# Optimization experiments

Measured on AMD Instinct MI355X. Metric: run time of the kernel, lower is better.

The kernel has to match this reference:

```python
import jax, jax.numpy as jnp
import numpy as np

B, N, T, D, O = 8, 1024, 12, 64, 64

def setup_inputs() -> dict:
    key = jax.random.key(0)
    k1, k2, k3 = jax.random.split(key, 3)
    x = jax.random.normal(k1, (B, N, T, D), dtype=jnp.float32)
    # row-normalized random adjacency (dense mask, as in the torch module)
    adj = jax.random.uniform(k2, (N, N), dtype=jnp.float32)
    norm_adj = adj / jnp.sum(adj, axis=-1, keepdims=True)
    theta_w = jax.random.normal(k3, (D, O), dtype=jnp.float32) / np.sqrt(D)
    return {"x": x, "norm_adj": norm_adj, "theta_w": theta_w}

def reference(x, norm_adj, theta_w):
    b, n, t, d = x.shape
    # [B, N, T, D] -> [B*T, N, D]
    xr = jnp.transpose(x, (0, 2, 1, 3)).reshape(b * t, n, d)
    # spatial attention scores [B*T, N, N]
    scores = jnp.einsum('gnd,gmd->gnm', xr, xr) / jnp.sqrt(jnp.float32(d))
    attn = jax.nn.softmax(scores, axis=-1)
    # adjacency-masked attention, then aggregate and project
    agg = jnp.einsum('gnm,gmd->gnd', norm_adj[None, :, :] * attn, xr)
    out = jnp.einsum('gnd,do->gno', agg, theta_w)
    # [B*T, N, O] -> [B, N, T, O], relu
    out = jnp.transpose(out.reshape(b, t, n, -1), (0, 2, 1, 3))
    return jax.nn.relu(out)
```

## Files before the change

kernel.cpp:

```cpp
#include <hip/hip_runtime.h>


#define NB    8
#define NT    12
#define NNODE 1024
#define ND    64
#define XROW  768
#define NG    96

typedef __bf16 bf16x8 __attribute__((ext_vector_type(8)));
typedef __bf16 bf16x4 __attribute__((ext_vector_type(4)));
typedef float  floatx4 __attribute__((ext_vector_type(4)));

#define MFMA(a,b,c) __builtin_amdgcn_mfma_f32_16x16x32_bf16((a),(b),(c),0,0,0)

#define QSCALE 0.18033688011112042f

#define KSTRIDE 72
#define VSTRIDE 40
#define PSTRIDE 36
#define AGSTRIDE 68
#define OFF_KHI 0
#define OFF_KLO 4608
#define OFF_VHI 9216
#define OFF_VLO 14336
#define OFF_P   19456
#define SMEM_BYTES (19456 + 128*PSTRIDE*4)

#define WXHI  0
#define WXLO  6291456
#define WXTHI 12582912
#define WXTLO 18874368
#define WTHI  25165824
#define WTLO  25169920
#define WS_BYTES 50348032ULL

struct bfpair { __bf16 h, l; };

__device__ __forceinline__ bfpair split1(float f) {
    bfpair r;
    __bf16 hb = (__bf16)f;
    float hf = __builtin_bit_cast(float,
                   (unsigned)__builtin_bit_cast(unsigned short, hb) << 16);
    r.h = hb;
    r.l = (__bf16)(f - hf);
    return r;
}

__global__ void __launch_bounds__(256)
presplit(const float* __restrict__ x, const float* __restrict__ theta,
         __bf16* __restrict__ ws)
{
    __shared__ __align__(16) float T[64 * 68];
    const int tid  = threadIdx.x;
    const int bx   = blockIdx.x;
    const int g    = bx >> 4;
    const int nblk = bx & 15;
    const int bb   = g / NT;
    const int tt   = g - bb * NT;
    const int n0   = nblk * 64;

    __bf16* Xhi  = ws + WXHI  + (size_t)g * 65536;
    __bf16* Xlo  = ws + WXLO  + (size_t)g * 65536;
    __bf16* XThi = ws + WXTHI + (size_t)g * 65536;
    __bf16* XTlo = ws + WXTLO + (size_t)g * 65536;
    const float* xg = x + (size_t)bb * (NNODE * XROW) + (size_t)tt * ND;

    #pragma unroll
    for (int i = 0; i < 4; ++i) {
        int chunk = i * 256 + tid;
        int n  = chunk >> 4;
        int c4 = (chunk & 15) * 4;
        floatx4 f = *(const floatx4*)(xg + (size_t)(n0 + n) * XROW + c4);
        *(floatx4*)(T + n * 68 + c4) = f;
        bf16x4 h, l;
        #pragma unroll
        for (int j = 0; j < 4; ++j) {
            bfpair p = split1(f[j]); h[j] = p.h; l[j] = p.l;
        }
        *(bf16x4*)(Xhi + (size_t)(n0 + n) * 64 + c4) = h;
        *(bf16x4*)(Xlo + (size_t)(n0 + n) * 64 + c4) = l;
    }
    __syncthreads();

    {
        const int d  = tid >> 2;
        const int nc = (tid & 3) * 16;
        bf16x8 h0, l0, h1, l1;
        #pragma unroll
        for (int j = 0; j < 8; ++j) {
            bfpair p = split1(T[(nc + j) * 68 + d]);     h0[j] = p.h; l0[j] = p.l;
            bfpair q = split1(T[(nc + 8 + j) * 68 + d]); h1[j] = q.h; l1[j] = q.l;
        }
        __bf16* dsth = XThi + (size_t)d * NNODE + n0 + nc;
        __bf16* dstl = XTlo + (size_t)d * NNODE + n0 + nc;
        *(bf16x8*)dsth = h0; *(bf16x8*)(dsth + 8) = h1;
        *(bf16x8*)dstl = l0; *(bf16x8*)(dstl + 8) = l1;
    }

    if (bx < 2) {
        int c  = bx * 256 + tid;
        int o  = c >> 3;
        int d0 = (c & 7) * 8;
        bf16x8 h, l;
        #pragma unroll
        for (int i = 0; i < 8; ++i) {
            bfpair p = split1(theta[(size_t)(d0 + i) * ND + o]);
            h[i] = p.h; l[i] = p.l;
        }
        *(bf16x8*)(ws + WTHI + (size_t)o * 64 + d0) = h;
        *(bf16x8*)(ws + WTLO + (size_t)o * 64 + d0) = l;
    }
}

__global__ void __launch_bounds__(256, 3)
spattn4(const __bf16* __restrict__ ws, const float* __restrict__ adj,
        float* __restrict__ out)
{
    __shared__ __align__(16) char smem[SMEM_BYTES];
    __bf16* Khi = (__bf16*)(smem + OFF_KHI);
    __bf16* Klo = (__bf16*)(smem + OFF_KLO);
    __bf16* Vhi = (__bf16*)(smem + OFF_VHI);
    __bf16* Vlo = (__bf16*)(smem + OFF_VLO);
    float*  Pm  = (float*)(smem + OFF_P);

    const int tid  = threadIdx.x;
    const int wave = tid >> 6;
    const int lane = tid & 63;
    const int l16  = lane & 15;
    const int quad = lane >> 4;

    const int bx   = blockIdx.x;
    const int g    = bx % NG;
    const int rblk = bx / NG;
    const int bb   = g / NT;
    const int tt   = g - bb * NT;
    const int row0 = rblk * 128;

    const __bf16* xh  = ws + WXHI  + (size_t)g * 65536;
    const __bf16* xl  = ws + WXLO  + (size_t)g * 65536;
    const __bf16* xth = ws + WXTHI + (size_t)g * 65536;
    const __bf16* xtl = ws + WXTLO + (size_t)g * 65536;

    bf16x8 qhi[2][2], qlo[2][2];
    #pragma unroll
    for (int mt = 0; mt < 2; ++mt) {
        const __bf16* q0 = xh + (size_t)(row0 + wave*32 + mt*16 + l16) * 64 + quad*8;
        const __bf16* q1 = xl + (size_t)(row0 + wave*32 + mt*16 + l16) * 64 + quad*8;
        #pragma unroll
        for (int ks = 0; ks < 2; ++ks) {
            qhi[mt][ks] = *(const bf16x8*)(q0 + ks*32);
            qlo[mt][ks] = *(const bf16x8*)(q1 + ks*32);
        }
    }

    const floatx4 vzero = {0.f, 0.f, 0.f, 0.f};
    floatx4 acc[2][4];
    #pragma unroll
    for (int mt = 0; mt < 2; ++mt)
        #pragma unroll
        for (int dt = 0; dt < 4; ++dt)
            acc[mt][dt] = vzero;
    float lpart[2][4] = {{0.f,0.f,0.f,0.f},{0.f,0.f,0.f,0.f}};

    const int skey = tid >> 3;
    const int sd0  = (tid & 7) * 8;
    const int svd  = tid >> 2;
    const int svk0 = (tid & 3) * 8;

    bf16x8 kh, kl, vhs, vls;
    kh  = *(const bf16x8*)(xh  + (size_t)skey * 64 + sd0);
    kl  = *(const bf16x8*)(xl  + (size_t)skey * 64 + sd0);
    vhs = *(const bf16x8*)(xth + (size_t)svd * NNODE + svk0);
    vls = *(const bf16x8*)(xtl + (size_t)svd * NNODE + svk0);

    for (int ct = 0; ct < 32; ++ct) {
        const int key0 = ct * 32;
        __syncthreads();
        *(bf16x8*)(Khi + skey*KSTRIDE + sd0) = kh;
        *(bf16x8*)(Klo + skey*KSTRIDE + sd0) = kl;
        *(bf16x8*)(Vhi + svd*VSTRIDE + svk0) = vhs;
        *(bf16x8*)(Vlo + svd*VSTRIDE + svk0) = vls;
        __syncthreads();
        if (ct < 31) {
            const int nk = key0 + 32;
            kh  = *(const bf16x8*)(xh  + (size_t)(nk + skey) * 64 + sd0);
            kl  = *(const bf16x8*)(xl  + (size_t)(nk + skey) * 64 + sd0);
            vhs = *(const bf16x8*)(xth + (size_t)svd * NNODE + nk + svk0);
            vls = *(const bf16x8*)(xtl + (size_t)svd * NNODE + nk + svk0);
        }
        float av[2][2][4];
        #pragma unroll
        for (int mt = 0; mt < 2; ++mt)
            #pragma unroll
            for (int nt = 0; nt < 2; ++nt)
                #pragma unroll
                for (int r = 0; r < 4; ++r)
                    av[mt][nt][r] = adj[(size_t)(row0 + wave*32 + mt*16 + quad*4 + r) * NNODE
                                        + key0 + nt*16 + l16];

        floatx4 S[2][2] = {{vzero, vzero}, {vzero, vzero}};
        #pragma unroll
        for (int ks = 0; ks < 2; ++ks) {
            #pragma unroll
            for (int nt = 0; nt < 2; ++nt) {
                bf16x8 bh = *(const bf16x8*)(Khi + (nt*16 + l16)*KSTRIDE + ks*32 + quad*8);
                bf16x8 bl = *(const bf16x8*)(Klo + (nt*16 + l16)*KSTRIDE + ks*32 + quad*8);
                #pragma unroll
                for (int mt = 0; mt < 2; ++mt) {
                    S[mt][nt] = MFMA(qhi[mt][ks], bh, S[mt][nt]);
                    S[mt][nt] = MFMA(qlo[mt][ks], bh, S[mt][nt]);
                    S[mt][nt] = MFMA(qhi[mt][ks], bl, S[mt][nt]);
                }
            }
        }
        #pragma unroll
        for (int mt = 0; mt < 2; ++mt)
            #pragma unroll
            for (int nt = 0; nt < 2; ++nt)
                #pragma unroll
                for (int r = 0; r < 4; ++r) {
                    float w = __builtin_amdgcn_exp2f(S[mt][nt][r] * QSCALE);
                    lpart[mt][r] += w;
                    Pm[(wave*32 + mt*16 + quad*4 + r)*PSTRIDE + nt*16 + l16] = av[mt][nt][r] * w;
                }
        bf16x8 pah[2], pal[2];
        #pragma unroll
        for (int mt = 0; mt < 2; ++mt) {
            const float* pp = Pm + (wave*32 + mt*16 + l16)*PSTRIDE + quad*8;
            floatx4 p0 = *(const floatx4*)pp;
            floatx4 p1 = *(const floatx4*)(pp + 4);
            #pragma unroll
            for (int i = 0; i < 4; ++i) {
                bfpair q0 = split1(p0[i]); pah[mt][i]   = q0.h; pal[mt][i]   = q0.l;
                bfpair q1 = split1(p1[i]); pah[mt][4+i] = q1.h; pal[mt][4+i] = q1.l;
            }
        }
        #pragma unroll
        for (int dt = 0; dt < 4; ++dt) {
            bf16x8 vvh = *(const bf16x8*)(Vhi + (dt*16 + l16)*VSTRIDE + quad*8);
            bf16x8 vvl = *(const bf16x8*)(Vlo + (dt*16 + l16)*VSTRIDE + quad*8);
            #pragma unroll
            for (int mt = 0; mt < 2; ++mt) {
                acc[mt][dt] = MFMA(pah[mt], vvh, acc[mt][dt]);
                acc[mt][dt] = MFMA(pal[mt], vvh, acc[mt][dt]);
                acc[mt][dt] = MFMA(pah[mt], vvl, acc[mt][dt]);
            }
        }
    }

    float linv[2][4];
    #pragma unroll
    for (int mt = 0; mt < 2; ++mt)
        #pragma unroll
        for (int r = 0; r < 4; ++r) {
            float lv = lpart[mt][r];
            lv += __shfl_xor(lv, 1);
            lv += __shfl_xor(lv, 2);
            lv += __shfl_xor(lv, 4);
            lv += __shfl_xor(lv, 8);
            linv[mt][r] = 1.0f / lv;
        }

    __syncthreads();
    float* AG = (float*)smem;
    #pragma unroll
    for (int mt = 0; mt < 2; ++mt)
        #pragma unroll
        for (int dt = 0; dt < 4; ++dt)
            #pragma unroll
            for (int r = 0; r < 4; ++r)
                AG[(wave*32 + mt*16 + quad*4 + r)*AGSTRIDE + dt*16 + l16]
                    = acc[mt][dt][r] * linv[mt][r];

    const __bf16* Th = ws + WTHI;
    const __bf16* Tl = ws + WTLO;
    bf16x8 th[4][2], tlw[4][2];
    #pragma unroll
    for (int ot = 0; ot < 4; ++ot)
        #pragma unroll
        for (int ks = 0; ks < 2; ++ks) {
            th[ot][ks]  = *(const bf16x8*)(Th + (size_t)(ot*16 + l16)*64 + ks*32 + quad*8);
            tlw[ot][ks] = *(const bf16x8*)(Tl + (size_t)(ot*16 + l16)*64 + ks*32 + quad*8);
        }

    floatx4 oacc[2][4];
    #pragma unroll
    for (int mt = 0; mt < 2; ++mt)
        #pragma unroll
        for (int ot = 0; ot < 4; ++ot)
            oacc[mt][ot] = vzero;
    __syncthreads();
    #pragma unroll
    for (int ks = 0; ks < 2; ++ks) {
        bf16x8 ah[2], al[2];
        #pragma unroll
        for (int mt = 0; mt < 2; ++mt) {
            const float* ap = AG + (wave*32 + mt*16 + l16)*AGSTRIDE + ks*32 + quad*8;
            floatx4 a0 = *(const floatx4*)ap;
            floatx4 a1 = *(const floatx4*)(ap + 4);
            #pragma unroll
            for (int i = 0; i < 4; ++i) {
                bfpair q0 = split1(a0[i]); ah[mt][i]   = q0.h; al[mt][i]   = q0.l;
                bfpair q1 = split1(a1[i]); ah[mt][4+i] = q1.h; al[mt][4+i] = q1.l;
            }
        }
        #pragma unroll
        for (int ot = 0; ot < 4; ++ot)
            #pragma unroll
            for (int mt = 0; mt < 2; ++mt) {
                oacc[mt][ot] = MFMA(ah[mt], th[ot][ks], oacc[mt][ot]);
                oacc[mt][ot] = MFMA(al[mt], th[ot][ks], oacc[mt][ot]);
                oacc[mt][ot] = MFMA(ah[mt], tlw[ot][ks], oacc[mt][ot]);
            }
    }

    float* obase = out + (size_t)bb * (NNODE * XROW) + tt * ND;
    #pragma unroll
    for (int mt = 0; mt < 2; ++mt)
        #pragma unroll
        for (int ot = 0; ot < 4; ++ot)
            #pragma unroll
            for (int r = 0; r < 4; ++r) {
                float v = oacc[mt][ot][r];
                obase[(size_t)(row0 + wave*32 + mt*16 + quad*4 + r) * XROW + ot*16 + l16]
                    = v > 0.f ? v : 0.f;
            }
}

__global__ void __launch_bounds__(256, 2)
spattn_fb(const float* __restrict__ x, const float* __restrict__ adj,
          const float* __restrict__ theta, float* __restrict__ out)
{
    __shared__ __align__(16) char smem[SMEM_BYTES];
    __bf16* Khi = (__bf16*)(smem + OFF_KHI);
    __bf16* Klo = (__bf16*)(smem + OFF_KLO);
    __bf16* Vhi = (__bf16*)(smem + OFF_VHI);
    __bf16* Vlo = (__bf16*)(smem + OFF_VLO);
    float*  Pm  = (float*)(smem + OFF_P);

    const int tid  = threadIdx.x;
    const int wave = tid >> 6;
    const int lane = tid & 63;
    const int l16  = lane & 15;
    const int quad = lane >> 4;

    const int bx   = blockIdx.x;
    const int g    = bx >> 3;
    const int rblk = bx & 7;
    const int bb   = g / NT;
    const int tt   = g - bb * NT;
    const int row0 = rblk * 128;

    const float* xbase = x + (size_t)bb * (NNODE * XROW) + tt * ND;

    bf16x8 qhi[2][2], qlo[2][2];
    #pragma unroll
    for (int mt = 0; mt < 2; ++mt) {
        const float* qsrc = xbase + (size_t)(row0 + wave*32 + mt*16 + l16) * XROW;
        #pragma unroll
        for (int ks = 0; ks < 2; ++ks) {
            floatx4 f0 = *(const floatx4*)(qsrc + ks*32 + quad*8);
            floatx4 f1 = *(const floatx4*)(qsrc + ks*32 + quad*8 + 4);
            #pragma unroll
            for (int i = 0; i < 4; ++i) {
                bfpair p0 = split1(f0[i]*QSCALE);
                qhi[mt][ks][i]   = p0.h; qlo[mt][ks][i]   = p0.l;
                bfpair p1 = split1(f1[i]*QSCALE);
                qhi[mt][ks][4+i] = p1.h; qlo[mt][ks][4+i] = p1.l;
            }
        }
    }

    const floatx4 vzero = {0.f, 0.f, 0.f, 0.f};
    floatx4 acc[2][4];
    #pragma unroll
    for (int mt = 0; mt < 2; ++mt)
        #pragma unroll
        for (int dt = 0; dt < 4; ++dt)
            acc[mt][dt] = vzero;
    float lpart[2][4] = {{0.f,0.f,0.f,0.f},{0.f,0.f,0.f,0.f}};

    const int skey = tid >> 3;
    const int sd0  = (tid & 7) * 8;
    const int svd  = tid >> 2;
    const int svk0 = (tid & 3) * 8;
    floatx4 kf0, kf1;
    float vf[8];

    {
        const float* ksrc = xbase + (size_t)skey * XROW + sd0;
        kf0 = *(const floatx4*)ksrc;
        kf1 = *(const floatx4*)(ksrc + 4);
        const float* vsrc = xbase + (size_t)svk0 * XROW + svd;
        #pragma unroll
        for (int i = 0; i < 8; ++i) vf[i] = vsrc[i * XROW];
    }

    for (int ct = 0; ct < 32; ++ct) {
        const int key0 = ct * 32;
        __syncthreads();
        {
            bf16x8 h, l;
            #pragma unroll
            for (int i = 0; i < 4; ++i) {
                bfpair p0 = split1(kf0[i]); h[i]   = p0.h; l[i]   = p0.l;
                bfpair p1 = split1(kf1[i]); h[4+i] = p1.h; l[4+i] = p1.l;
            }
            *(bf16x8*)(Khi + skey*KSTRIDE + sd0) = h;
            *(bf16x8*)(Klo + skey*KSTRIDE + sd0) = l;
            bf16x8 vh, vl;
            #pragma unroll
            for (int i = 0; i < 8; ++i) {
                bfpair p = split1(vf[i]); vh[i] = p.h; vl[i] = p.l;
            }
            *(bf16x8*)(Vhi + svd*VSTRIDE + svk0) = vh;
            *(bf16x8*)(Vlo + svd*VSTRIDE + svk0) = vl;
        }
        __syncthreads();
        if (ct < 31) {
            const int nk = key0 + 32;
            const float* ksrc = xbase + (size_t)(nk + skey) * XROW + sd0;
            kf0 = *(const floatx4*)ksrc;
            kf1 = *(const floatx4*)(ksrc + 4);
            const float* vsrc = xbase + (size_t)(nk + svk0) * XROW + svd;
            #pragma unroll
            for (int i = 0; i < 8; ++i) vf[i] = vsrc[i * XROW];
        }
        float av[2][2][4];
        #pragma unroll
        for (int mt = 0; mt < 2; ++mt)
            #pragma unroll
            for (int nt = 0; nt < 2; ++nt)
                #pragma unroll
                for (int r = 0; r < 4; ++r)
                    av[mt][nt][r] = adj[(size_t)(row0 + wave*32 + mt*16 + quad*4 + r) * NNODE
                                        + key0 + nt*16 + l16];

        floatx4 S[2][2] = {{vzero, vzero}, {vzero, vzero}};
        #pragma unroll
        for (int ks = 0; ks < 2; ++ks) {
            #pragma unroll
            for (int nt = 0; nt < 2; ++nt) {
                bf16x8 bh = *(const bf16x8*)(Khi + (nt*16 + l16)*KSTRIDE + ks*32 + quad*8);
                bf16x8 bl = *(const bf16x8*)(Klo + (nt*16 + l16)*KSTRIDE + ks*32 + quad*8);
                #pragma unroll
                for (int mt = 0; mt < 2; ++mt) {
                    S[mt][nt] = MFMA(qhi[mt][ks], bh, S[mt][nt]);
                    S[mt][nt] = MFMA(qlo[mt][ks], bh, S[mt][nt]);
                    S[mt][nt] = MFMA(qhi[mt][ks], bl, S[mt][nt]);
                }
            }
        }
        #pragma unroll
        for (int mt = 0; mt < 2; ++mt)
            #pragma unroll
            for (int nt = 0; nt < 2; ++nt)
                #pragma unroll
                for (int r = 0; r < 4; ++r) {
                    float w = __builtin_amdgcn_exp2f(S[mt][nt][r]);
                    lpart[mt][r] += w;
                    Pm[(wave*32 + mt*16 + quad*4 + r)*PSTRIDE + nt*16 + l16] = av[mt][nt][r] * w;
                }
        bf16x8 pah[2], pal[2];
        #pragma unroll
        for (int mt = 0; mt < 2; ++mt) {
            const float* pp = Pm + (wave*32 + mt*16 + l16)*PSTRIDE + quad*8;
            floatx4 p0 = *(const floatx4*)pp;
            floatx4 p1 = *(const floatx4*)(pp + 4);
            #pragma unroll
            for (int i = 0; i < 4; ++i) {
                bfpair q0 = split1(p0[i]); pah[mt][i]   = q0.h; pal[mt][i]   = q0.l;
                bfpair q1 = split1(p1[i]); pah[mt][4+i] = q1.h; pal[mt][4+i] = q1.l;
            }
        }
        #pragma unroll
        for (int dt = 0; dt < 4; ++dt) {
            bf16x8 vh = *(const bf16x8*)(Vhi + (dt*16 + l16)*VSTRIDE + quad*8);
            bf16x8 vl = *(const bf16x8*)(Vlo + (dt*16 + l16)*VSTRIDE + quad*8);
            #pragma unroll
            for (int mt = 0; mt < 2; ++mt) {
                acc[mt][dt] = MFMA(pah[mt], vh, acc[mt][dt]);
                acc[mt][dt] = MFMA(pal[mt], vh, acc[mt][dt]);
                acc[mt][dt] = MFMA(pah[mt], vl, acc[mt][dt]);
            }
        }
    }

    float linv[2][4];
    #pragma unroll
    for (int mt = 0; mt < 2; ++mt)
        #pragma unroll
        for (int r = 0; r < 4; ++r) {
            float lv = lpart[mt][r];
            lv += __shfl_xor(lv, 1);
            lv += __shfl_xor(lv, 2);
            lv += __shfl_xor(lv, 4);
            lv += __shfl_xor(lv, 8);
            linv[mt][r] = 1.0f / lv;
        }

    __syncthreads();
    float* AG = (float*)smem;
    #pragma unroll
    for (int mt = 0; mt < 2; ++mt)
        #pragma unroll
        for (int dt = 0; dt < 4; ++dt)
            #pragma unroll
            for (int r = 0; r < 4; ++r)
                AG[(wave*32 + mt*16 + quad*4 + r)*AGSTRIDE + dt*16 + l16]
                    = acc[mt][dt][r] * linv[mt][r];

    bf16x8 th[4][2], tl[4][2];
    #pragma unroll
    for (int ot = 0; ot < 4; ++ot)
        #pragma unroll
        for (int ks = 0; ks < 2; ++ks)
            #pragma unroll
            for (int j = 0; j < 8; ++j) {
                float tv = theta[(ks*32 + quad*8 + j)*ND + ot*16 + l16];
                bfpair p = split1(tv);
                th[ot][ks][j] = p.h; tl[ot][ks][j] = p.l;
            }

    floatx4 oacc[2][4];
    #pragma unroll
    for (int mt = 0; mt < 2; ++mt)
        #pragma unroll
        for (int ot = 0; ot < 4; ++ot)
            oacc[mt][ot] = vzero;
    __syncthreads();
    #pragma unroll
    for (int ks = 0; ks < 2; ++ks) {
        bf16x8 ah[2], al[2];
        #pragma unroll
        for (int mt = 0; mt < 2; ++mt) {
            const float* ap = AG + (wave*32 + mt*16 + l16)*AGSTRIDE + ks*32 + quad*8;
            floatx4 a0 = *(const floatx4*)ap;
            floatx4 a1 = *(const floatx4*)(ap + 4);
            #pragma unroll
            for (int i = 0; i < 4; ++i) {
                bfpair q0 = split1(a0[i]); ah[mt][i]   = q0.h; al[mt][i]   = q0.l;
                bfpair q1 = split1(a1[i]); ah[mt][4+i] = q1.h; al[mt][4+i] = q1.l;
            }
        }
        #pragma unroll
        for (int ot = 0; ot < 4; ++ot)
            #pragma unroll
            for (int mt = 0; mt < 2; ++mt) {
                oacc[mt][ot] = MFMA(ah[mt], th[ot][ks], oacc[mt][ot]);
                oacc[mt][ot] = MFMA(al[mt], th[ot][ks], oacc[mt][ot]);
                oacc[mt][ot] = MFMA(ah[mt], tl[ot][ks], oacc[mt][ot]);
            }
    }

    float* obase = out + (size_t)bb * (NNODE * XROW) + tt * ND;
    #pragma unroll
    for (int mt = 0; mt < 2; ++mt)
        #pragma unroll
        for (int ot = 0; ot < 4; ++ot)
            #pragma unroll
            for (int r = 0; r < 4; ++r) {
                float v = oacc[mt][ot][r];
                obase[(size_t)(row0 + wave*32 + mt*16 + quad*4 + r) * XROW + ot*16 + l16]
                    = v > 0.f ? v : 0.f;
            }
}

extern "C" void kernel_launch(void* const* d_in, const int* in_sizes, int n_in,
                              void* d_out, int out_size, void* d_ws, size_t ws_size,
                              hipStream_t stream) {
    (void)in_sizes; (void)n_in; (void)out_size;
    const float* x     = (const float*)d_in[0];
    const float* adj   = (const float*)d_in[1];
    const float* theta = (const float*)d_in[2];
    float* out = (float*)d_out;
    if (d_ws != nullptr && ws_size >= WS_BYTES) {
        __bf16* ws = (__bf16*)d_ws;
        presplit<<<dim3(1536), dim3(256), 0, stream>>>(x, theta, ws);
        spattn4<<<dim3(768), dim3(256), 0, stream>>>(ws, adj, out);
    } else {
        spattn_fb<<<dim3(768), dim3(256), 0, stream>>>(x, adj, theta, out);
    }
}
```

Measured before the change: 172.6 us.

## Compute transposed scores to feed P to PV MFMA from registers

Swaps the MFMA operand order so the score tile comes out transposed, which lets each lane's exp-weighted, adjacency-scaled values be packed straight into the A operand of the PV MFMA. This removes the shared-memory round-trip through the P buffer. To make that work, presplit now writes V with a permuted key order that matches the new register layout. Adjacency reads become 16-byte vector loads, the row-sum reduction is restructured, and the smaller shared footprint allows a launch bound of 4 blocks per CU. The risks are extra register pressure and correctness depending on the permutation matching the MFMA layout exactly.

```diff
diff --git a/kernel.cpp b/kernel.cpp
--- a/kernel.cpp
+++ b/kernel.cpp
@@ -18,19 +18,20 @@
 
 #define KSTRIDE 72
 #define VSTRIDE 40
-#define PSTRIDE 36
 #define AGSTRIDE 68
 #define OFF_KHI 0
 #define OFF_KLO 4608
 #define OFF_VHI 9216
 #define OFF_VLO 14336
+#define SMEM5   (128 * AGSTRIDE * 4)
+#define PSTRIDE 36
+#define SMEM_FB (19456 + 128*PSTRIDE*4)
 #define OFF_P   19456
-#define SMEM_BYTES (19456 + 128*PSTRIDE*4)
 
 #define WXHI  0
 #define WXLO  6291456
-#define WXTHI 12582912
-#define WXTLO 18874368
+#define WVPHI 12582912
+#define WVPLO 18874368
 #define WTHI  25165824
 #define WTLO  25169920
 #define WS_BYTES 50348032ULL
@@ -62,8 +63,8 @@
 
     __bf16* Xhi  = ws + WXHI  + (size_t)g * 65536;
     __bf16* Xlo  = ws + WXLO  + (size_t)g * 65536;
-    __bf16* XThi = ws + WXTHI + (size_t)g * 65536;
-    __bf16* XTlo = ws + WXTLO + (size_t)g * 65536;
+    __bf16* VPhi = ws + WVPHI + (size_t)g * 65536;
+    __bf16* VPlo = ws + WVPLO + (size_t)g * 65536;
     const float* xg = x + (size_t)bb * (NNODE * XROW) + (size_t)tt * ND;
 
     #pragma unroll
@@ -86,14 +87,21 @@
     {
         const int d  = tid >> 2;
         const int nc = (tid & 3) * 16;
+        const int tb = nc & 32;
         bf16x8 h0, l0, h1, l1;
         #pragma unroll
         for (int j = 0; j < 8; ++j) {
-            bfpair p = split1(T[(nc + j) * 68 + d]);     h0[j] = p.h; l0[j] = p.l;
-            bfpair q = split1(T[(nc + 8 + j) * 68 + d]); h1[j] = q.h; l1[j] = q.l;
-        }
-        __bf16* dsth = XThi + (size_t)d * NNODE + n0 + nc;
-        __bf16* dstl = XTlo + (size_t)d * NNODE + n0 + nc;
+            int c0 = (nc & 31) + j;
+            int k0 = ((c0 & 7) >> 2) * 16 + (c0 >> 3) * 4 + (c0 & 3);
+            bfpair p = split1(T[(tb + k0) * 68 + d]);
+            h0[j] = p.h; l0[j] = p.l;
+            int c1 = (nc & 31) + 8 + j;
+            int k1 = ((c1 & 7) >> 2) * 16 + (c1 >> 3) * 4 + (c1 & 3);
+            bfpair q = split1(T[(tb + k1) * 68 + d]);
+            h1[j] = q.h; l1[j] = q.l;
+        }
+        __bf16* dsth = VPhi + (size_t)d * NNODE + n0 + nc;
+        __bf16* dstl = VPlo + (size_t)d * NNODE + n0 + nc;
         *(bf16x8*)dsth = h0; *(bf16x8*)(dsth + 8) = h1;
         *(bf16x8*)dstl = l0; *(bf16x8*)(dstl + 8) = l1;
     }
@@ -113,16 +121,15 @@
     }
 }
 
-__global__ void __launch_bounds__(256, 3)
-spattn4(const __bf16* __restrict__ ws, const float* __restrict__ adj,
+__global__ void __launch_bounds__(256, 4)
+spattn5(const __bf16* __restrict__ ws, const float* __restrict__ adj,
         float* __restrict__ out)
 {
-    __shared__ __align__(16) char smem[SMEM_BYTES];
+    __shared__ __align__(16) char smem[SMEM5];
     __bf16* Khi = (__bf16*)(smem + OFF_KHI);
     __bf16* Klo = (__bf16*)(smem + OFF_KLO);
     __bf16* Vhi = (__bf16*)(smem + OFF_VHI);
     __bf16* Vlo = (__bf16*)(smem + OFF_VLO);
-    float*  Pm  = (float*)(smem + OFF_P);
 
     const int tid  = threadIdx.x;
     const int wave = tid >> 6;
@@ -139,8 +146,8 @@
 
     const __bf16* xh  = ws + WXHI  + (size_t)g * 65536;
     const __bf16* xl  = ws + WXLO  + (size_t)g * 65536;
-    const __bf16* xth = ws + WXTHI + (size_t)g * 65536;
-    const __bf16* xtl = ws + WXTLO + (size_t)g * 65536;
+    const __bf16* vph = ws + WVPHI + (size_t)g * 65536;
+    const __bf16* vpl = ws + WVPLO + (size_t)g * 65536;
 
     bf16x8 qhi[2][2], qlo[2][2];
     #pragma unroll
@@ -161,7 +168,7 @@
         #pragma unroll
         for (int dt = 0; dt < 4; ++dt)
             acc[mt][dt] = vzero;
-    float lpart[2][4] = {{0.f,0.f,0.f,0.f},{0.f,0.f,0.f,0.f}};
+    float lpart[2] = {0.f, 0.f};
 
     const int skey = tid >> 3;
     const int sd0  = (tid & 7) * 8;
@@ -171,8 +178,8 @@
     bf16x8 kh, kl, vhs, vls;
     kh  = *(const bf16x8*)(xh  + (size_t)skey * 64 + sd0);
     kl  = *(const bf16x8*)(xl  + (size_t)skey * 64 + sd0);
-    vhs = *(const bf16x8*)(xth + (size_t)svd * NNODE + svk0);
-    vls = *(const bf16x8*)(xtl + (size_t)svd * NNODE + svk0);
+    vhs = *(const bf16x8*)(vph + (size_t)svd * NNODE + svk0);
+    vls = *(const bf16x8*)(vpl + (size_t)svd * NNODE + svk0);
 
     for (int ct = 0; ct < 32; ++ct) {
         const int key0 = ct * 32;
@@ -186,34 +193,35 @@
             const int nk = key0 + 32;
             kh  = *(const bf16x8*)(xh  + (size_t)(nk + skey) * 64 + sd0);
             kl  = *(const bf16x8*)(xl  + (size_t)(nk + skey) * 64 + sd0);
-            vhs = *(const bf16x8*)(xth + (size_t)svd * NNODE + nk + svk0);
-            vls = *(const bf16x8*)(xtl + (size_t)svd * NNODE + nk + svk0);
-        }
-        float av[2][2][4];
+            vhs = *(const bf16x8*)(vph + (size_t)svd * NNODE + nk + svk0);
+            vls = *(const bf16x8*)(vpl + (size_t)svd * NNODE + nk + svk0);
+        }
+        floatx4 av[2][2];
         #pragma unroll
         for (int mt = 0; mt < 2; ++mt)
             #pragma unroll
             for (int nt = 0; nt < 2; ++nt)
-                #pragma unroll
-                for (int r = 0; r < 4; ++r)
-                    av[mt][nt][r] = adj[(size_t)(row0 + wave*32 + mt*16 + quad*4 + r) * NNODE
-                                        + key0 + nt*16 + l16];
+                av[mt][nt] = *(const floatx4*)(adj
+                    + (size_t)(row0 + wave*32 + mt*16 + l16) * NNODE
+                    + key0 + nt*16 + quad*4);
 
         floatx4 S[2][2] = {{vzero, vzero}, {vzero, vzero}};
         #pragma unroll
         for (int ks = 0; ks < 2; ++ks) {
             #pragma unroll
             for (int nt = 0; nt < 2; ++nt) {
-                bf16x8 bh = *(const bf16x8*)(Khi + (nt*16 + l16)*KSTRIDE + ks*32 + quad*8);
-                bf16x8 bl = *(const bf16x8*)(Klo + (nt*16 + l16)*KSTRIDE + ks*32 + quad*8);
+                bf16x8 ah = *(const bf16x8*)(Khi + (nt*16 + l16)*KSTRIDE + ks*32 + quad*8);
+                bf16x8 al = *(const bf16x8*)(Klo + (nt*16 + l16)*KSTRIDE + ks*32 + quad*8);
                 #pragma unroll
                 for (int mt = 0; mt < 2; ++mt) {
-                    S[mt][nt] = MFMA(qhi[mt][ks], bh, S[mt][nt]);
-                    S[mt][nt] = MFMA(qlo[mt][ks], bh, S[mt][nt]);
-                    S[mt][nt] = MFMA(qhi[mt][ks], bl, S[mt][nt]);
+                    S[mt][nt] = MFMA(ah, qhi[mt][ks], S[mt][nt]);
+                    S[mt][nt] = MFMA(ah, qlo[mt][ks], S[mt][nt]);
+                    S[mt][nt] = MFMA(al, qhi[mt][ks], S[mt][nt]);
                 }
             }
         }
+
+        bf16x8 pah[2], pal[2];
         #pragma unroll
         for (int mt = 0; mt < 2; ++mt)
             #pragma unroll
@@ -221,21 +229,12 @@
                 #pragma unroll
                 for (int r = 0; r < 4; ++r) {
                     float w = __builtin_amdgcn_exp2f(S[mt][nt][r] * QSCALE);
-                    lpart[mt][r] += w;
-                    Pm[(wave*32 + mt*16 + quad*4 + r)*PSTRIDE + nt*16 + l16] = av[mt][nt][r] * w;
+                    lpart[mt] += w;
+                    bfpair pp = split1(av[mt][nt][r] * w);
+                    pah[mt][nt*4 + r] = pp.h;
+                    pal[mt][nt*4 + r] = pp.l;
                 }
-        bf16x8 pah[2], pal[2];
-        #pragma unroll
-        for (int mt = 0; mt < 2; ++mt) {
-            const float* pp = Pm + (wave*32 + mt*16 + l16)*PSTRIDE + quad*8;
-            floatx4 p0 = *(const floatx4*)pp;
-            floatx4 p1 = *(const floatx4*)(pp + 4);
-            #pragma unroll
-            for (int i = 0; i < 4; ++i) {
-                bfpair q0 = split1(p0[i]); pah[mt][i]   = q0.h; pal[mt][i]   = q0.l;
-                bfpair q1 = split1(p1[i]); pah[mt][4+i] = q1.h; pal[mt][4+i] = q1.l;
-            }
-        }
+
         #pragma unroll
         for (int dt = 0; dt < 4; ++dt) {
             bf16x8 vvh = *(const bf16x8*)(Vhi + (dt*16 + l16)*VSTRIDE + quad*8);
@@ -251,16 +250,14 @@
 
     float linv[2][4];
     #pragma unroll
-    for (int mt = 0; mt < 2; ++mt)
-        #pragma unroll
-        for (int r = 0; r < 4; ++r) {
-            float lv = lpart[mt][r];
-            lv += __shfl_xor(lv, 1);
-            lv += __shfl_xor(lv, 2);
-            lv += __shfl_xor(lv, 4);
-            lv += __shfl_xor(lv, 8);
-            linv[mt][r] = 1.0f / lv;
-        }
+    for (int mt = 0; mt < 2; ++mt) {
+        float lv = lpart[mt];
+        lv += __shfl_xor(lv, 16);
+        lv += __shfl_xor(lv, 32);
+        #pragma unroll
+        for (int r = 0; r < 4; ++r)
+            linv[mt][r] = 1.0f / __shfl(lv, quad*4 + r);
+    }
 
     __syncthreads();
     float* AG = (float*)smem;
@@ -332,7 +329,7 @@
 spattn_fb(const float* __restrict__ x, const float* __restrict__ adj,
           const float* __restrict__ theta, float* __restrict__ out)
 {
-    __shared__ __align__(16) char smem[SMEM_BYTES];
+    __shared__ __align__(16) char smem[SMEM_FB];
     __bf16* Khi = (__bf16*)(smem + OFF_KHI);
     __bf16* Klo = (__bf16*)(smem + OFF_KLO);
     __bf16* Vhi = (__bf16*)(smem + OFF_VHI);
@@ -578,7 +575,7 @@
     if (d_ws != nullptr && ws_size >= WS_BYTES) {
         __bf16* ws = (__bf16*)d_ws;
         presplit<<<dim3(1536), dim3(256), 0, stream>>>(x, theta, ws);
-        spattn4<<<dim3(768), dim3(256), 0, stream>>>(ws, adj, out);
+        spattn5<<<dim3(768), dim3(256), 0, stream>>>(ws, adj, out);
     } else {
         spattn_fb<<<dim3(768), dim3(256), 0, stream>>>(x, adj, theta, out);
     }
```

New measurement: 171.5 us. About the same (-0.6%).
